# Kernel optimization log

Hardware: AMD Instinct MI355X
Metric: run time of the kernel (lower is better)

Reference implementation:

```python
import jax, jax.numpy as jnp
import numpy as np

N, E, F, H, L, G = 200000, 400000, 128, 128, 3, 4096
BN_EPS = 1e-5


def setup_inputs() -> dict:
    key = jax.random.key(0)
    ks = jax.random.split(key, 8)
    x = jax.random.normal(ks[0], (N, F), dtype=jnp.float32)
    edge_index = jax.random.randint(ks[1], (2, E), 0, N, dtype=jnp.int64)
    batch = jnp.sort(jax.random.randint(ks[2], (N,), 0, G, dtype=jnp.int64))
    s = 1.0 / np.sqrt(H)
    W_in = (jax.random.normal(ks[3], (F, H), jnp.float32) * s)
    b_in = jnp.zeros((H,), jnp.float32)
    W_conv = (jax.random.normal(ks[4], (L, H, H), jnp.float32) * s)
    b_conv = jnp.zeros((L, H), jnp.float32)
    gamma = jnp.ones((L, H), jnp.float32)
    beta = jnp.zeros((L, H), jnp.float32)
    W_out = (jax.random.normal(ks[5], (H, H), jnp.float32) * s)
    b_out = jnp.zeros((H,), jnp.float32)
    return dict(x=x, W_in=W_in, b_in=b_in, W_conv=W_conv, b_conv=b_conv,
                gamma=gamma, beta=beta, W_out=W_out, b_out=b_out,
                edge_index=edge_index, batch=batch)


def reference(x, W_in, b_in, W_conv, b_conv, gamma, beta, W_out, b_out,
              edge_index, batch):
    # --- GCN normalization (PyG GCNConv with self-loops, symmetric norm) ---
    loops = jnp.arange(N, dtype=edge_index.dtype)
    row = jnp.concatenate([edge_index[0], loops])  # source nodes
    col = jnp.concatenate([edge_index[1], loops])  # target nodes
    deg = jax.ops.segment_sum(jnp.ones_like(col, x.dtype), col, num_segments=N)
    dinv = jnp.where(deg > 0, jax.lax.rsqrt(deg), 0.0)
    norm = dinv[row] * dinv[col]                   # [E+N]

    h = x @ W_in + b_in                            # [N, H]
    for i in range(L):
        # GCNConv: linear -> gather -> normalize -> scatter-add -> bias
        msg = (h @ W_conv[i])[row] * norm[:, None]
        hn = jax.ops.segment_sum(msg, col, num_segments=N) + b_conv[i]
        # BatchNorm1d (batch statistics, as in training) + ReLU, residual
        mu = hn.mean(axis=0)
        var = hn.var(axis=0)
        hn = (hn - mu) * jax.lax.rsqrt(var + BN_EPS) * gamma[i] + beta[i]
        h = h + jax.nn.relu(hn)

    # global_mean_pool over batch assignment
    ssum = jax.ops.segment_sum(h, batch, num_segments=G)
    cnt = jax.ops.segment_sum(jnp.ones((N,), h.dtype), batch, num_segments=G)
    g = ssum / jnp.clip(cnt, 1.0)[:, None]         # [G, H]
    return g @ W_out + b_out
```

## Files before the change

### kernel.cpp

```cpp
#include <hip/hip_runtime.h>

#define NN 200000
#define NE 400000
#define HD 128
#define NL 3
#define NG 4096
#define BN_EPS 1e-5f

#define OFF_DINV  0UL
#define OFF_H     800000UL
#define OFF_U     103200000UL
#define OFF_ACC   205600000UL
#define OFF_POOL  308000000UL
#define OFF_GSTART 310097152UL
#define OFF_CSUM  310113540UL
#define OFF_CSQ   310115076UL
#define OFF_SCALE 310116612UL
#define OFF_SHIFT 310117124UL
#define OFF_CNTI  310117636UL
#define OFF_OFFS  310917636UL
#define OFF_CUR   311717652UL
#define OFF_SRCS  312517652UL
#define OFF_BSUM  314117652UL

#define SCAN_B 196

typedef __attribute__((ext_vector_type(8))) short v8s;
typedef __attribute__((ext_vector_type(4))) float v4f;
typedef __attribute__((ext_vector_type(4))) unsigned short v4u;
typedef __attribute__((ext_vector_type(8))) unsigned short v8u;

__device__ inline unsigned short f_to_bf_rne(float f) {
    unsigned u = __float_as_uint(f);
    return (unsigned short)((u + 0x7fffu + ((u >> 16) & 1u)) >> 16);
}

__device__ inline v4f bf4_to_f(v4u a) {
    v4f r;
    r[0] = __uint_as_float(((unsigned)a[0]) << 16);
    r[1] = __uint_as_float(((unsigned)a[1]) << 16);
    r[2] = __uint_as_float(((unsigned)a[2]) << 16);
    r[3] = __uint_as_float(((unsigned)a[3]) << 16);
    return r;
}

__global__ void count_deg_i(const int* __restrict__ col, int* __restrict__ cnt) {
    int e = blockIdx.x * blockDim.x + threadIdx.x;
    if (e < NE) atomicAdd(&cnt[col[e]], 1);
}

__global__ void finalize_dinv(const int* __restrict__ cnt, float* __restrict__ dinv) {
    int i = blockIdx.x * blockDim.x + threadIdx.x;
    if (i < NN) dinv[i] = rsqrtf((float)(cnt[i] + 1));
}

__global__ void scan_phase1(const int* __restrict__ cnt, int* __restrict__ bsum) {
    __shared__ int sh[256];
    int b = blockIdx.x, t = threadIdx.x;
    int base = b * 1024 + t * 4;
    int s = 0;
#pragma unroll
    for (int j = 0; j < 4; ++j) if (base + j < NN) s += cnt[base + j];
    sh[t] = s;
    __syncthreads();
    for (int st = 128; st > 0; st >>= 1) {
        if (t < st) sh[t] += sh[t + st];
        __syncthreads();
    }
    if (t == 0) bsum[b] = sh[0];
}

__global__ void scan_phase2(int* __restrict__ bsum, int* __restrict__ offs) {
    if (threadIdx.x == 0) {
        int run = 0;
        for (int i = 0; i < SCAN_B; ++i) { int v = bsum[i]; bsum[i] = run; run += v; }
        offs[NN] = NE;
    }
}

__global__ void scan_phase3(const int* __restrict__ cnt, const int* __restrict__ bsum,
                            int* __restrict__ offs) {
    __shared__ int sh[256];
    int b = blockIdx.x, t = threadIdx.x;
    int base = b * 1024 + t * 4;
    int v[4];
    int s = 0;
#pragma unroll
    for (int j = 0; j < 4; ++j) { v[j] = (base + j < NN) ? cnt[base + j] : 0; s += v[j]; }
    sh[t] = s;
    __syncthreads();
    for (int st = 1; st < 256; st <<= 1) {
        int x = (t >= st) ? sh[t - st] : 0;
        __syncthreads();
        sh[t] += x;
        __syncthreads();
    }
    int run = sh[t] - s + bsum[b];
#pragma unroll
    for (int j = 0; j < 4; ++j) {
        if (base + j < NN) { offs[base + j] = run; run += v[j]; }
    }
}

__global__ void fill_csr(const int* __restrict__ row, const int* __restrict__ col,
                         const int* __restrict__ offs, int* __restrict__ cur,
                         int* __restrict__ srcs) {
    int e = blockIdx.x * blockDim.x + threadIdx.x;
    if (e >= NE) return;
    int c = col[e];
    int p = offs[c] + atomicAdd(&cur[c], 1);
    srcs[p] = row[e];
}

__device__ inline void cvt_split(float f, short& hi, short& lo) {
    unsigned u = __float_as_uint(f);
    unsigned rh = (u + 0x7fffu + ((u >> 16) & 1u)) >> 16;
    hi = (short)rh;
    float fh = __uint_as_float(rh << 16);
    float d = f - fh;
    unsigned u2 = __float_as_uint(d);
    unsigned rl = (u2 + 0x7fffu + ((u2 >> 16) & 1u)) >> 16;
    lo = (short)rl;
}

#define GEMM_BLOCKS 512
template <bool ADD_BIAS, bool SCALE_DINV, bool FUSE_BN, bool OUT_BF16>
__launch_bounds__(512, 4)
__global__ void gemm_mfma(float* __restrict__ A, const float* __restrict__ W,
                          const float* __restrict__ bias, const float* __restrict__ dinv,
                          const float* __restrict__ bnscale, const float* __restrict__ bnshift,
                          const unsigned short* __restrict__ bnacc,
                          void* __restrict__ Ov, int M) {
    __shared__ short Wh[HD * HD];
    __shared__ short Wlo[HD * HD];

    {
        int c = threadIdx.x >> 2;
        int quarter = threadIdx.x & 3;
#pragma unroll
        for (int g8 = 0; g8 < 4; ++g8) {
            int G = quarter * 4 + g8;
            v8s h8, l8;
#pragma unroll
            for (int j = 0; j < 8; ++j) {
                float f = W[(G * 8 + j) * HD + c];
                short hi, lo;
                cvt_split(f, hi, lo);
                h8[j] = hi; l8[j] = lo;
            }
            int off = c * HD + (G ^ (c & 7)) * 8;
            *(v8s*)&Wh[off] = h8;
            *(v8s*)&Wlo[off] = l8;
        }
    }
    __syncthreads();

    int wave = threadIdx.x >> 6;
    int lane = threadIdx.x & 63;
    int m = lane & 15;
    int q = lane >> 4;

    const float4* sc4 = (const float4*)bnscale;
    const float4* sf4 = (const float4*)bnshift;

    for (int task = blockIdx.x; task * 128 < M; task += GEMM_BLOCKS) {
        int rbase = task * 128 + wave * 16;
        if (rbase >= M) continue;

        float* Ar = A + (size_t)(rbase + m) * HD;

        v8s ah[4], al[4];
#pragma unroll
        for (int kc = 0; kc < 4; ++kc) {
            float4 x0 = *(const float4*)(Ar + kc * 32 + q * 8);
            float4 x1 = *(const float4*)(Ar + kc * 32 + q * 8 + 4);
            if (FUSE_BN) {
                v8u y8 = *(const v8u*)(bnacc + (size_t)(rbase + m) * HD + kc * 32 + q * 8);
                v4u ya = {y8[0], y8[1], y8[2], y8[3]};
                v4u yb = {y8[4], y8[5], y8[6], y8[7]};
                v4f y0 = bf4_to_f(ya);
                v4f y1 = bf4_to_f(yb);
                float4 s0 = sc4[kc * 8 + q * 2], s1 = sc4[kc * 8 + q * 2 + 1];
                float4 f0 = sf4[kc * 8 + q * 2], f1 = sf4[kc * 8 + q * 2 + 1];
                x0.x += fmaxf(fmaf(y0[0], s0.x, f0.x), 0.f);
                x0.y += fmaxf(fmaf(y0[1], s0.y, f0.y), 0.f);
                x0.z += fmaxf(fmaf(y0[2], s0.z, f0.z), 0.f);
                x0.w += fmaxf(fmaf(y0[3], s0.w, f0.w), 0.f);
                x1.x += fmaxf(fmaf(y1[0], s1.x, f1.x), 0.f);
                x1.y += fmaxf(fmaf(y1[1], s1.y, f1.y), 0.f);
                x1.z += fmaxf(fmaf(y1[2], s1.z, f1.z), 0.f);
                x1.w += fmaxf(fmaf(y1[3], s1.w, f1.w), 0.f);
                *(float4*)(Ar + kc * 32 + q * 8) = x0;
                *(float4*)(Ar + kc * 32 + q * 8 + 4) = x1;
            }
            float xs[8] = {x0.x, x0.y, x0.z, x0.w, x1.x, x1.y, x1.z, x1.w};
            v8s h8, l8;
#pragma unroll
            for (int j = 0; j < 8; ++j) {
                short hi, lo;
                cvt_split(xs[j], hi, lo);
                h8[j] = hi; l8[j] = lo;
            }
            ah[kc] = h8; al[kc] = l8;
        }

        v4f acc[8];
#pragma unroll
        for (int ct = 0; ct < 8; ++ct) acc[ct] = (v4f){0.f, 0.f, 0.f, 0.f};

#pragma unroll
        for (int kc = 0; kc < 4; ++kc) {
#pragma unroll
            for (int ct = 0; ct < 8; ++ct) {
                int c = ct * 16 + m;
                int off = c * HD + (((kc * 4 + q) ^ (c & 7)) * 8);
                v8s bh = *(const v8s*)&Wh[off];
                v8s bl = *(const v8s*)&Wlo[off];
                acc[ct] = __builtin_amdgcn_mfma_f32_16x16x32_bf16(ah[kc], bh, acc[ct], 0, 0, 0);
                acc[ct] = __builtin_amdgcn_mfma_f32_16x16x32_bf16(al[kc], bh, acc[ct], 0, 0, 0);
                acc[ct] = __builtin_amdgcn_mfma_f32_16x16x32_bf16(ah[kc], bl, acc[ct], 0, 0, 0);
            }
        }

        float dv[4];
#pragma unroll
        for (int reg = 0; reg < 4; ++reg)
            dv[reg] = SCALE_DINV ? dinv[rbase + q * 4 + reg] : 1.0f;
#pragma unroll
        for (int ct = 0; ct < 8; ++ct) {
            int colb = ct * 16 + m;
            float bb = ADD_BIAS ? bias[colb] : 0.0f;
#pragma unroll
            for (int reg = 0; reg < 4; ++reg) {
                int rr = rbase + q * 4 + reg;
                float v = acc[ct][reg] + bb;
                if (SCALE_DINV) v *= dv[reg];
                if (OUT_BF16) {
                    ((unsigned short*)Ov)[(size_t)rr * HD + colb] = f_to_bf_rne(v);
                } else {
                    ((float*)Ov)[(size_t)rr * HD + colb] = v;
                }
            }
        }
    }
}

#define GATHER_BLOCKS 1024
__global__ void gather_bn(const int* __restrict__ offs, const int* __restrict__ srcs,
                          const unsigned short* __restrict__ u, const float* __restrict__ dinv,
                          unsigned short* __restrict__ acc,
                          float* __restrict__ colsum, float* __restrict__ colsumsq) {
    const v8u* u8p = (const v8u*)u;
    v8u* acc8 = (v8u*)acc;
    int n = threadIdx.x >> 4;
    int q = threadIdx.x & 15;
    v4f t1a = (v4f){0.f, 0.f, 0.f, 0.f}, t1b = t1a;
    v4f t2a = t1a, t2b = t1a;

    for (int node = blockIdx.x * 16 + n; node < NN; node += GATHER_BLOCKS * 16) {
        v8u s8 = u8p[(size_t)node * 16 + q];
        v4f sa = bf4_to_f((v4u){s8[0], s8[1], s8[2], s8[3]});
        v4f sb = bf4_to_f((v4u){s8[4], s8[5], s8[6], s8[7]});
        int k = offs[node];
        int k1 = offs[node + 1];
        for (; k + 2 <= k1; k += 2) {
            int s0 = srcs[k], s1 = srcs[k + 1];
            v8u a8 = u8p[(size_t)s0 * 16 + q];
            v8u b8 = u8p[(size_t)s1 * 16 + q];
            sa += bf4_to_f((v4u){a8[0], a8[1], a8[2], a8[3]});
            sb += bf4_to_f((v4u){a8[4], a8[5], a8[6], a8[7]});
            sa += bf4_to_f((v4u){b8[0], b8[1], b8[2], b8[3]});
            sb += bf4_to_f((v4u){b8[4], b8[5], b8[6], b8[7]});
        }
        if (k < k1) {
            v8u a8 = u8p[(size_t)srcs[k] * 16 + q];
            sa += bf4_to_f((v4u){a8[0], a8[1], a8[2], a8[3]});
            sb += bf4_to_f((v4u){a8[4], a8[5], a8[6], a8[7]});
        }
        float d = dinv[node];
        sa *= d; sb *= d;
        v8u o8;
        o8[0] = f_to_bf_rne(sa[0]); o8[1] = f_to_bf_rne(sa[1]);
        o8[2] = f_to_bf_rne(sa[2]); o8[3] = f_to_bf_rne(sa[3]);
        o8[4] = f_to_bf_rne(sb[0]); o8[5] = f_to_bf_rne(sb[1]);
        o8[6] = f_to_bf_rne(sb[2]); o8[7] = f_to_bf_rne(sb[3]);
        acc8[(size_t)node * 16 + q] = o8;
        v4f ra = bf4_to_f((v4u){o8[0], o8[1], o8[2], o8[3]});
        v4f rb = bf4_to_f((v4u){o8[4], o8[5], o8[6], o8[7]});
        t1a += ra; t1b += rb;
        t2a += ra * ra; t2b += rb * rb;
    }

    __shared__ float sh1[16][HD];
    __shared__ float sh2[16][HD];
    *(v4f*)&sh1[n][q * 8] = t1a;
    *(v4f*)&sh1[n][q * 8 + 4] = t1b;
    *(v4f*)&sh2[n][q * 8] = t2a;
    *(v4f*)&sh2[n][q * 8 + 4] = t2b;
    __syncthreads();
    if (threadIdx.x < HD) {
        int c = threadIdx.x;
        float a1 = 0.f, a2 = 0.f;
#pragma unroll
        for (int i = 0; i < 16; ++i) { a1 += sh1[i][c]; a2 += sh2[i][c]; }
        atomicAdd(&colsum[c], a1);
        atomicAdd(&colsumsq[c], a2);
    }
}

__global__ void bn_finalize(const float* __restrict__ colsum, const float* __restrict__ colsumsq,
                            const float* __restrict__ gamma, const float* __restrict__ beta,
                            float* __restrict__ scale, float* __restrict__ shift) {
    int c = threadIdx.x;
    float invn = 1.0f / (float)NN;
    float m = colsum[c] * invn;
    float v = colsumsq[c] * invn - m * m;
    float sc = gamma[c] * rsqrtf(v + BN_EPS);
    scale[c] = sc;
    shift[c] = beta[c] - m * sc;
}

__global__ void group_bounds(const int* __restrict__ batch, int* __restrict__ gstart) {
    int g = blockIdx.x * blockDim.x + threadIdx.x;
    if (g > NG) return;
    if (g == NG) { gstart[NG] = NN; return; }
    int lo = 0, hi = NN;
    while (lo < hi) {
        int mid = (lo + hi) >> 1;
        if (batch[mid] < g) lo = mid + 1; else hi = mid;
    }
    gstart[g] = lo;
}

__launch_bounds__(128)
__global__ void pool_bn_mean(const unsigned short* __restrict__ acc, const float* __restrict__ h,
                             const float* __restrict__ scale, const float* __restrict__ shift,
                             const int* __restrict__ gstart, float* __restrict__ pool) {
    int g = blockIdx.x;
    int c = threadIdx.x;
    float sc = scale[c], sf = shift[c];
    int s = gstart[g], e = gstart[g + 1];
    float a = 0.f;
    for (int r = s; r < e; ++r) {
        float yv = __uint_as_float(((unsigned)acc[(size_t)r * HD + c]) << 16);
        float y = fmaxf(fmaf(yv, sc, sf), 0.f);
        a += h[(size_t)r * HD + c] + y;
    }
    float ic = 1.0f / fmaxf((float)(e - s), 1.0f);
    pool[(size_t)g * HD + c] = a * ic;
}

__launch_bounds__(128)
__global__ void out_gemm(const float* __restrict__ pool,
                         const float* __restrict__ Wout, const float* __restrict__ bout,
                         float* __restrict__ out) {
    __shared__ float hb[HD];
    int g = blockIdx.x;
    int c = threadIdx.x;
    hb[c] = pool[(size_t)g * HD + c];
    __syncthreads();
    float o = bout[c];
#pragma unroll 8
    for (int k = 0; k < HD; ++k) o = fmaf(hb[k], Wout[k * HD + c], o);
    out[(size_t)g * HD + c] = o;
}

extern "C" void kernel_launch(void* const* d_in, const int* in_sizes, int n_in,
                              void* d_out, int out_size, void* d_ws, size_t ws_size,
                              hipStream_t stream) {
    const float* x      = (const float*)d_in[0];
    const float* W_in   = (const float*)d_in[1];
    const float* b_in   = (const float*)d_in[2];
    const float* W_conv = (const float*)d_in[3];
    const float* gamma  = (const float*)d_in[5];
    const float* beta   = (const float*)d_in[6];
    const float* W_out  = (const float*)d_in[7];
    const float* b_out  = (const float*)d_in[8];
    const int*   edge   = (const int*)d_in[9];
    const int*   batch  = (const int*)d_in[10];
    float* out = (float*)d_out;

    char* ws = (char*)d_ws;
    float* dinv   = (float*)(ws + OFF_DINV);
    float* h      = (float*)(ws + OFF_H);
    unsigned short* u   = (unsigned short*)(ws + OFF_U);
    unsigned short* acc = (unsigned short*)(ws + OFF_ACC);
    float* pool   = (float*)(ws + OFF_POOL);
    int*   gstart = (int*)(ws + OFF_GSTART);
    float* csum   = (float*)(ws + OFF_CSUM);
    float* csq    = (float*)(ws + OFF_CSQ);
    float* scale  = (float*)(ws + OFF_SCALE);
    float* shift  = (float*)(ws + OFF_SHIFT);
    int*   cnti   = (int*)(ws + OFF_CNTI);
    int*   offs   = (int*)(ws + OFF_OFFS);
    int*   cur    = (int*)(ws + OFF_CUR);
    int*   srcs   = (int*)(ws + OFF_SRCS);
    int*   bsum   = (int*)(ws + OFF_BSUM);

    const int* row = edge;
    const int* col = edge + NE;

    hipMemsetAsync(ws + OFF_CSUM, 0, OFF_SHIFT + 512 - OFF_CSUM, stream);
    hipMemsetAsync(ws + OFF_CNTI, 0, OFF_SRCS - OFF_CNTI, stream);

    count_deg_i<<<(NE + 255) / 256, 256, 0, stream>>>(col, cnti);
    finalize_dinv<<<(NN + 255) / 256, 256, 0, stream>>>(cnti, dinv);
    scan_phase1<<<SCAN_B, 256, 0, stream>>>(cnti, bsum);
    scan_phase2<<<1, 64, 0, stream>>>(bsum, offs);
    scan_phase3<<<SCAN_B, 256, 0, stream>>>(cnti, bsum, offs);
    fill_csr<<<(NE + 255) / 256, 256, 0, stream>>>(row, col, offs, cur, srcs);
    group_bounds<<<(NG + 256) / 256, 256, 0, stream>>>(batch, gstart);

    gemm_mfma<true, false, false, false><<<GEMM_BLOCKS, 512, 0, stream>>>(
        (float*)x, W_in, b_in, nullptr, nullptr, nullptr, nullptr, h, NN);

    for (int l = 0; l < NL; ++l) {
        if (l == 0) {
            gemm_mfma<false, true, false, true><<<GEMM_BLOCKS, 512, 0, stream>>>(
                h, W_conv + (size_t)l * HD * HD, nullptr, dinv,
                nullptr, nullptr, nullptr, u, NN);
        } else {
            gemm_mfma<false, true, true, true><<<GEMM_BLOCKS, 512, 0, stream>>>(
                h, W_conv + (size_t)l * HD * HD, nullptr, dinv,
                scale, shift, acc, u, NN);
        }
        gather_bn<<<GATHER_BLOCKS, 256, 0, stream>>>(
            offs, srcs, u, dinv, acc, csum + l * HD, csq + l * HD);
        bn_finalize<<<1, HD, 0, stream>>>(
            csum + l * HD, csq + l * HD, gamma + l * HD, beta + l * HD, scale, shift);
    }

    pool_bn_mean<<<NG, 128, 0, stream>>>(acc, h, scale, shift, gstart, pool);
    out_gemm<<<NG, 128, 0, stream>>>(pool, W_out, b_out, out);
}
```

Measured before the change: 657.8 us.

## Store residual hidden state in bf16 and drop one MFMA pass for bf16 inputs

The residual stream h is now kept in bf16 instead of fp32. This halves its read and write traffic in the conv GEMMs and in the final pooling. For bf16 inputs the A operand needs no hi/lo split, so one of the three split MFMA passes is skipped and the GEMM does less compute. The cost is precision: every layer's residual accumulation is rounded to bf16, so error can build up across layers.

```diff
diff --git a/kernel.cpp b/kernel.cpp
--- a/kernel.cpp
+++ b/kernel.cpp
@@ -35,12 +35,14 @@
     return (unsigned short)((u + 0x7fffu + ((u >> 16) & 1u)) >> 16);
 }
 
+__device__ inline float bf_to_f(unsigned short a) {
+    return __uint_as_float(((unsigned)a) << 16);
+}
+
 __device__ inline v4f bf4_to_f(v4u a) {
     v4f r;
-    r[0] = __uint_as_float(((unsigned)a[0]) << 16);
-    r[1] = __uint_as_float(((unsigned)a[1]) << 16);
-    r[2] = __uint_as_float(((unsigned)a[2]) << 16);
-    r[3] = __uint_as_float(((unsigned)a[3]) << 16);
+    r[0] = bf_to_f(a[0]); r[1] = bf_to_f(a[1]);
+    r[2] = bf_to_f(a[2]); r[3] = bf_to_f(a[3]);
     return r;
 }
 
@@ -124,13 +126,13 @@
 }
 
 #define GEMM_BLOCKS 512
-template <bool ADD_BIAS, bool SCALE_DINV, bool FUSE_BN, bool OUT_BF16>
+template <bool ADD_BIAS, bool SCALE_DINV, bool FUSE_BN, bool A_BF16>
 __launch_bounds__(512, 4)
-__global__ void gemm_mfma(float* __restrict__ A, const float* __restrict__ W,
+__global__ void gemm_mfma(void* __restrict__ Av, const float* __restrict__ W,
                           const float* __restrict__ bias, const float* __restrict__ dinv,
                           const float* __restrict__ bnscale, const float* __restrict__ bnshift,
                           const unsigned short* __restrict__ bnacc,
-                          void* __restrict__ Ov, int M) {
+                          unsigned short* __restrict__ O, int M) {
     __shared__ short Wh[HD * HD];
     __shared__ short Wlo[HD * HD];
 
@@ -160,48 +162,45 @@
     int m = lane & 15;
     int q = lane >> 4;
 
-    const float4* sc4 = (const float4*)bnscale;
-    const float4* sf4 = (const float4*)bnshift;
-
     for (int task = blockIdx.x; task * 128 < M; task += GEMM_BLOCKS) {
         int rbase = task * 128 + wave * 16;
         if (rbase >= M) continue;
 
-        float* Ar = A + (size_t)(rbase + m) * HD;
-
         v8s ah[4], al[4];
 #pragma unroll
         for (int kc = 0; kc < 4; ++kc) {
-            float4 x0 = *(const float4*)(Ar + kc * 32 + q * 8);
-            float4 x1 = *(const float4*)(Ar + kc * 32 + q * 8 + 4);
-            if (FUSE_BN) {
-                v8u y8 = *(const v8u*)(bnacc + (size_t)(rbase + m) * HD + kc * 32 + q * 8);
-                v4u ya = {y8[0], y8[1], y8[2], y8[3]};
-                v4u yb = {y8[4], y8[5], y8[6], y8[7]};
-                v4f y0 = bf4_to_f(ya);
-                v4f y1 = bf4_to_f(yb);
-                float4 s0 = sc4[kc * 8 + q * 2], s1 = sc4[kc * 8 + q * 2 + 1];
-                float4 f0 = sf4[kc * 8 + q * 2], f1 = sf4[kc * 8 + q * 2 + 1];
-                x0.x += fmaxf(fmaf(y0[0], s0.x, f0.x), 0.f);
-                x0.y += fmaxf(fmaf(y0[1], s0.y, f0.y), 0.f);
-                x0.z += fmaxf(fmaf(y0[2], s0.z, f0.z), 0.f);
-                x0.w += fmaxf(fmaf(y0[3], s0.w, f0.w), 0.f);
-                x1.x += fmaxf(fmaf(y1[0], s1.x, f1.x), 0.f);
-                x1.y += fmaxf(fmaf(y1[1], s1.y, f1.y), 0.f);
-                x1.z += fmaxf(fmaf(y1[2], s1.z, f1.z), 0.f);
-                x1.w += fmaxf(fmaf(y1[3], s1.w, f1.w), 0.f);
-                *(float4*)(Ar + kc * 32 + q * 8) = x0;
-                *(float4*)(Ar + kc * 32 + q * 8 + 4) = x1;
+            if (!A_BF16) {
+                const float* Ar = (const float*)Av + (size_t)(rbase + m) * HD;
+                float4 x0 = *(const float4*)(Ar + kc * 32 + q * 8);
+                float4 x1 = *(const float4*)(Ar + kc * 32 + q * 8 + 4);
+                float xs[8] = {x0.x, x0.y, x0.z, x0.w, x1.x, x1.y, x1.z, x1.w};
+                v8s h8, l8;
+#pragma unroll
+                for (int j = 0; j < 8; ++j) {
+                    short hi, lo;
+                    cvt_split(xs[j], hi, lo);
+                    h8[j] = hi; l8[j] = lo;
+                }
+                ah[kc] = h8; al[kc] = l8;
+            } else {
+                unsigned short* Ar = (unsigned short*)Av + (size_t)(rbase + m) * HD;
+                v8u a8 = *(const v8u*)(Ar + kc * 32 + q * 8);
+                if (FUSE_BN) {
+                    v8u y8 = *(const v8u*)(bnacc + (size_t)(rbase + m) * HD + kc * 32 + q * 8);
+                    const float* scp = bnscale + kc * 32 + q * 8;
+                    const float* sfp = bnshift + kc * 32 + q * 8;
+                    v8u o8;
+#pragma unroll
+                    for (int j = 0; j < 8; ++j) {
+                        float hn = bf_to_f(a8[j]) +
+                                   fmaxf(fmaf(bf_to_f(y8[j]), scp[j], sfp[j]), 0.f);
+                        o8[j] = f_to_bf_rne(hn);
+                    }
+                    *(v8u*)(Ar + kc * 32 + q * 8) = o8;
+                    a8 = o8;
+                }
+                ah[kc] = (v8s)a8;
             }
-            float xs[8] = {x0.x, x0.y, x0.z, x0.w, x1.x, x1.y, x1.z, x1.w};
-            v8s h8, l8;
-#pragma unroll
-            for (int j = 0; j < 8; ++j) {
-                short hi, lo;
-                cvt_split(xs[j], hi, lo);
-                h8[j] = hi; l8[j] = lo;
-            }
-            ah[kc] = h8; al[kc] = l8;
         }
 
         v4f acc[8];
@@ -217,7 +216,8 @@
                 v8s bh = *(const v8s*)&Wh[off];
                 v8s bl = *(const v8s*)&Wlo[off];
                 acc[ct] = __builtin_amdgcn_mfma_f32_16x16x32_bf16(ah[kc], bh, acc[ct], 0, 0, 0);
-                acc[ct] = __builtin_amdgcn_mfma_f32_16x16x32_bf16(al[kc], bh, acc[ct], 0, 0, 0);
+                if (!A_BF16)
+                    acc[ct] = __builtin_amdgcn_mfma_f32_16x16x32_bf16(al[kc], bh, acc[ct], 0, 0, 0);
                 acc[ct] = __builtin_amdgcn_mfma_f32_16x16x32_bf16(ah[kc], bl, acc[ct], 0, 0, 0);
             }
         }
@@ -235,11 +235,7 @@
                 int rr = rbase + q * 4 + reg;
                 float v = acc[ct][reg] + bb;
                 if (SCALE_DINV) v *= dv[reg];
-                if (OUT_BF16) {
-                    ((unsigned short*)Ov)[(size_t)rr * HD + colb] = f_to_bf_rne(v);
-                } else {
-                    ((float*)Ov)[(size_t)rr * HD + colb] = v;
-                }
+                O[(size_t)rr * HD + colb] = f_to_bf_rne(v);
             }
         }
     }
@@ -333,7 +329,8 @@
 }
 
 __launch_bounds__(128)
-__global__ void pool_bn_mean(const unsigned short* __restrict__ acc, const float* __restrict__ h,
+__global__ void pool_bn_mean(const unsigned short* __restrict__ acc,
+                             const unsigned short* __restrict__ h,
                              const float* __restrict__ scale, const float* __restrict__ shift,
                              const int* __restrict__ gstart, float* __restrict__ pool) {
     int g = blockIdx.x;
@@ -342,9 +339,9 @@
     int s = gstart[g], e = gstart[g + 1];
     float a = 0.f;
     for (int r = s; r < e; ++r) {
-        float yv = __uint_as_float(((unsigned)acc[(size_t)r * HD + c]) << 16);
+        float yv = bf_to_f(acc[(size_t)r * HD + c]);
         float y = fmaxf(fmaf(yv, sc, sf), 0.f);
-        a += h[(size_t)r * HD + c] + y;
+        a += bf_to_f(h[(size_t)r * HD + c]) + y;
     }
     float ic = 1.0f / fmaxf((float)(e - s), 1.0f);
     pool[(size_t)g * HD + c] = a * ic;
@@ -382,7 +379,7 @@
 
     char* ws = (char*)d_ws;
     float* dinv   = (float*)(ws + OFF_DINV);
-    float* h      = (float*)(ws + OFF_H);
+    unsigned short* h   = (unsigned short*)(ws + OFF_H);
     unsigned short* u   = (unsigned short*)(ws + OFF_U);
     unsigned short* acc = (unsigned short*)(ws + OFF_ACC);
     float* pool   = (float*)(ws + OFF_POOL);
@@ -412,7 +409,7 @@
     group_bounds<<<(NG + 256) / 256, 256, 0, stream>>>(batch, gstart);
 
     gemm_mfma<true, false, false, false><<<GEMM_BLOCKS, 512, 0, stream>>>(
-        (float*)x, W_in, b_in, nullptr, nullptr, nullptr, nullptr, h, NN);
+        (void*)x, W_in, b_in, nullptr, nullptr, nullptr, nullptr, h, NN);
 
     for (int l = 0; l < NL; ++l) {
         if (l == 0) {
```

After: 600.9 us. 1.09x faster.
